# Optimization experiments

Measured on AMD Instinct MI355X. Metric: run time of the kernel, lower is better.

## Reference

```python
import jax, jax.numpy as jnp
import numpy as np

L, B, E, H = 1024, 8, 1024, 16
HD = E // H
SCALE = HD ** -0.5
EPS = 1e-5


def setup_inputs() -> dict:
    key = jax.random.key(0)
    ks = jax.random.split(key, 6)
    s = E ** -0.5
    return {
        "x": jax.random.normal(ks[0], (L, B, E), dtype=jnp.float32),
        "attn_mask": jnp.zeros((L, L), dtype=jnp.float32),
        "Wq": jax.random.normal(ks[1], (E, E), dtype=jnp.float32) * s,
        "bq": jnp.zeros((E,), dtype=jnp.float32),
        "Wk": jax.random.normal(ks[2], (E, E), dtype=jnp.float32) * s,
        "bk": jnp.zeros((E,), dtype=jnp.float32),
        "Wv": jax.random.normal(ks[3], (E, E), dtype=jnp.float32) * s,
        "bv": jnp.zeros((E,), dtype=jnp.float32),
        "Wo": jax.random.normal(ks[4], (E, E), dtype=jnp.float32) * s,
        "bo": jnp.zeros((E,), dtype=jnp.float32),
        "gamma": jnp.ones((E,), dtype=jnp.float32),
        "beta": jnp.zeros((E,), dtype=jnp.float32),
    }


def _layernorm(x, gamma, beta):
    mu = jnp.mean(x, axis=-1, keepdims=True)
    var = jnp.mean(jnp.square(x - mu), axis=-1, keepdims=True)
    return (x - mu) * jax.lax.rsqrt(var + EPS) * gamma + beta


def reference(x, attn_mask, Wq, bq, Wk, bk, Wv, bv, Wo, bo, gamma, beta):
    # x: (L, B, E); pre-LN residual attention block (dropout=0, eval)
    ln_x = _layernorm(x, gamma, beta)
    # torch Linear: y = x @ W.T + b
    q = (ln_x @ Wq.T + bq) * SCALE
    k = ln_x @ Wk.T + bk
    v = ln_x @ Wv.T + bv
    # (L, B, E) -> (B, H, L, hd)
    def split_heads(t):
        return t.reshape(L, B, H, HD).transpose(1, 2, 0, 3)
    q, k, v = split_heads(q), split_heads(k), split_heads(v)
    # full attention matrix, as in the original non-fused bmm path
    attn = jnp.einsum('bhqd,bhkd->bhqk', q, k) + attn_mask[None, None]
    attn = jax.nn.softmax(attn, axis=-1)
    out = jnp.einsum('bhqk,bhkd->bhqd', attn, v)  # (B, H, L, hd)
    out = out.transpose(2, 0, 1, 3).reshape(L, B, E)
    out = out @ Wo.T + bo
    return x + out
```

## Files before the change

kernel.cpp:

```cpp
#include <hip/hip_runtime.h>

#define LL 1024
#define BB 8
#define EE 1024
#define HH 16
#define HD 64
#define MROWS (LL*BB)

typedef __attribute__((ext_vector_type(8))) short short8v;
typedef __attribute__((ext_vector_type(4))) float f32x4;
typedef __attribute__((ext_vector_type(16))) float f32x16;

__device__ __forceinline__ unsigned short tobf(float f) {
    union { float f; unsigned u; } un; un.f = f;
    unsigned u = un.u;
    u += 0x7fffu + ((u >> 16) & 1u);
    return (unsigned short)(u >> 16);
}

__device__ __forceinline__ void load_lds16(const unsigned short* g, unsigned short* l) {
    __builtin_amdgcn_global_load_lds((const __attribute__((address_space(1))) unsigned int*)g,
                                     (__attribute__((address_space(3))) unsigned int*)l,
                                     16, 0, 0);
}

__global__ __launch_bounds__(256) void convw4_kernel(const float* __restrict__ w0,
                                                     const float* __restrict__ w1,
                                                     const float* __restrict__ w2,
                                                     const float* __restrict__ w3,
                                                     unsigned short* __restrict__ o0,
                                                     unsigned short* __restrict__ o1,
                                                     unsigned short* __restrict__ o2,
                                                     unsigned short* __restrict__ o3) {
    const float* w; unsigned short* o;
    switch (blockIdx.y) {
        case 0:  w = w0; o = o0; break;
        case 1:  w = w1; o = o1; break;
        case 2:  w = w2; o = o2; break;
        default: w = w3; o = o3; break;
    }
    int i = (blockIdx.x * 256 + threadIdx.x) * 4;
    float4 v = *(const float4*)&w[i];
    ushort4 r;
    r.x = tobf(v.x); r.y = tobf(v.y); r.z = tobf(v.z); r.w = tobf(v.w);
    *(ushort4*)&o[i] = r;
}

__global__ __launch_bounds__(256) void ln_kernel(const float* __restrict__ x,
                                                 const float* __restrict__ gamma,
                                                 const float* __restrict__ beta,
                                                 unsigned short* __restrict__ out) {
    const int row = blockIdx.x;
    const int tid = threadIdx.x;
    const float4 v = *(const float4*)&x[(size_t)row * EE + tid * 4];
    float s = v.x + v.y + v.z + v.w;
    float q = v.x*v.x + v.y*v.y + v.z*v.z + v.w*v.w;
    #pragma unroll
    for (int off = 1; off < 64; off <<= 1) {
        s += __shfl_xor(s, off);
        q += __shfl_xor(q, off);
    }
    __shared__ float ss[4], sq[4];
    const int wv = tid >> 6;
    if ((tid & 63) == 0) { ss[wv] = s; sq[wv] = q; }
    __syncthreads();
    s = ss[0] + ss[1] + ss[2] + ss[3];
    q = sq[0] + sq[1] + sq[2] + sq[3];
    const float mu = s * (1.0f / EE);
    const float var = q * (1.0f / EE) - mu * mu;
    const float rs = rsqrtf(var + 1e-5f);
    ushort4 o;
    o.x = tobf((v.x - mu) * rs * gamma[tid*4+0] + beta[tid*4+0]);
    o.y = tobf((v.y - mu) * rs * gamma[tid*4+1] + beta[tid*4+1]);
    o.z = tobf((v.z - mu) * rs * gamma[tid*4+2] + beta[tid*4+2]);
    o.w = tobf((v.w - mu) * rs * gamma[tid*4+3] + beta[tid*4+3]);
    *(ushort4*)&out[(size_t)row * EE + tid * 4] = o;
}

#define GEMM128_BODY(A_, W_)                                                              \
    __shared__ unsigned short a_sh[128*32];                                               \
    __shared__ unsigned short b_sh[128*32];                                               \
    const int tid = threadIdx.x, lane = tid & 63, wave = tid >> 6;                        \
    const int bm = blockIdx.y * 128, bn = blockIdx.x * 128;                               \
    const int wr = (wave >> 1) * 64, wc = (wave & 1) * 64;                                \
    const int l16 = lane & 15, lk8 = (lane >> 4) * 8;                                     \
    const int grow = lane >> 2, gcol = (lane & 3) * 8;                                    \
    f32x4 acc[4][4] = {};                                                                 \
    for (int k0 = 0; k0 < EE; k0 += 32) {                                                 \
        _Pragma("unroll")                                                                 \
        for (int i = 0; i < 2; ++i) {                                                     \
            const int c = wave * 2 + i;                                                   \
            load_lds16(&A_[(size_t)(bm + c*16 + grow)*EE + k0 + gcol], a_sh + c*512);     \
            load_lds16(&W_[(size_t)(bn + c*16 + grow)*EE + k0 + gcol], b_sh + c*512);     \
        }                                                                                 \
        __syncthreads();                                                                  \
        short8v af[4], bf[4];                                                             \
        _Pragma("unroll")                                                                 \
        for (int mi = 0; mi < 4; ++mi) af[mi] = *(const short8v*)&a_sh[(wr + mi*16 + l16)*32 + lk8]; \
        _Pragma("unroll")                                                                 \
        for (int ni = 0; ni < 4; ++ni) bf[ni] = *(const short8v*)&b_sh[(wc + ni*16 + l16)*32 + lk8]; \
        _Pragma("unroll")                                                                 \
        for (int mi = 0; mi < 4; ++mi)                                                    \
            _Pragma("unroll")                                                             \
            for (int ni = 0; ni < 4; ++ni)                                                \
                acc[mi][ni] = __builtin_amdgcn_mfma_f32_16x16x32_bf16(af[mi], bf[ni], acc[mi][ni], 0, 0, 0); \
        __syncthreads();                                                                  \
    }

__global__ __launch_bounds__(256) void gemm_qkv(const unsigned short* __restrict__ A,
                                                const unsigned short* __restrict__ W,
                                                const float* __restrict__ bq,
                                                const float* __restrict__ bk,
                                                const float* __restrict__ bv,
                                                unsigned short* __restrict__ qo,
                                                unsigned short* __restrict__ ko,
                                                unsigned short* __restrict__ vo) {
    GEMM128_BODY(A, W)
    const int seg = blockIdx.x >> 3;
    const float* bias = seg == 0 ? bq : (seg == 1 ? bk : bv);
    #pragma unroll
    for (int mi = 0; mi < 4; ++mi) {
        #pragma unroll
        for (int ni = 0; ni < 4; ++ni) {
            #pragma unroll
            for (int r = 0; r < 4; ++r) {
                const int m  = bm + wr + mi*16 + (lane >> 4)*4 + r;
                const int nn = (bn & 1023) + wc + ni*16 + l16;
                const float v = acc[mi][ni][r] + bias[nn];
                const int l = m >> 3, b = m & 7, h = nn >> 6, d = nn & 63;
                if (seg == 0)      qo[((size_t)(b*HH + h) * LL + l) * HD + d] = tobf(v * 0.125f);
                else if (seg == 1) ko[((size_t)(b*HH + h) * LL + l) * HD + d] = tobf(v);
                else               vo[((size_t)(b*HH + h) * HD + d) * LL + l] = tobf(v);
            }
        }
    }
}

__global__ __launch_bounds__(256) void gemm_o(const unsigned short* __restrict__ A,
                                              const unsigned short* __restrict__ W,
                                              const float* __restrict__ bias,
                                              const float* __restrict__ xres,
                                              float* __restrict__ outf) {
    GEMM128_BODY(A, W)
    #pragma unroll
    for (int mi = 0; mi < 4; ++mi) {
        #pragma unroll
        for (int ni = 0; ni < 4; ++ni) {
            #pragma unroll
            for (int r = 0; r < 4; ++r) {
                const int m = bm + wr + mi*16 + (lane >> 4)*4 + r;
                const int n = bn + wc + ni*16 + l16;
                outf[(size_t)m * EE + n] = acc[mi][ni][r] + bias[n] + xres[(size_t)m * EE + n];
            }
        }
    }
}

__global__ __launch_bounds__(256) void attn_kernel(const unsigned short* __restrict__ qarr,
                                                   const unsigned short* __restrict__ karr,
                                                   const unsigned short* __restrict__ vtarr,
                                                   const float* __restrict__ mask,
                                                   unsigned short* __restrict__ attn_out) {
    __shared__ __attribute__((aligned(16))) unsigned short k_sh[2][64*64];
    __shared__ __attribute__((aligned(16))) unsigned short v_sh[2][64*64];
    const int tid = threadIdx.x, lane = tid & 63, wave = tid >> 6;
    const int l32 = lane & 31, hi = lane >> 5;
    const int bh = blockIdx.y;
    const int qtok = blockIdx.x * 128 + wave * 32 + l32;
    const unsigned short* qb = qarr  + (size_t)bh * LL * HD;
    const unsigned short* kb = karr  + (size_t)bh * LL * HD;
    const unsigned short* vb = vtarr + (size_t)bh * HD * LL;

    short8v qf[4];
    #pragma unroll
    for (int dc = 0; dc < 4; ++dc)
        qf[dc] = *(const short8v*)&qb[(size_t)qtok * HD + dc*16 + hi*8];

    f32x16 acc[2] = {};
    float mrun = -1e30f, srun = 0.f;

    auto stage = [&](int buf, int kv) {
        #pragma unroll
        for (int i = 0; i < 2; ++i) {
            const int r = wave*16 + i*8 + (lane >> 3);
            const int c = ((lane & 7) ^ (r & 7)) * 8;
            load_lds16(&kb[(size_t)(kv + r) * HD + c], &k_sh[buf][(wave*16 + i*8) * 64]);
            load_lds16(&vb[(size_t)r * LL + kv + c],   &v_sh[buf][(wave*16 + i*8) * 64]);
        }
    };

    stage(0, 0);
    for (int t = 0; t < LL/64; ++t) {
        const int buf = t & 1;
        __syncthreads();
        if (t < LL/64 - 1) stage(buf ^ 1, (t + 1) * 64);

        #pragma unroll
        for (int sub = 0; sub < 2; ++sub) {
            f32x16 s = {};
            #pragma unroll
            for (int dc = 0; dc < 4; ++dc) {
                const int row = sub*32 + l32;
                const short8v kf = *(const short8v*)((const char*)&k_sh[buf][0]
                                     + (size_t)row*128 + (((dc*2 + hi) ^ (l32 & 7)) * 16));
                s = __builtin_amdgcn_mfma_f32_32x32x16_bf16(kf, qf[dc], s, 0, 0, 0);
            }
            const float* mrow = &mask[(size_t)qtok * LL + t*64 + sub*32 + hi*4];
            #pragma unroll
            for (int g = 0; g < 4; ++g) {
                const float4 mv = *(const float4*)&mrow[g*8];
                s[4*g+0] += mv.x; s[4*g+1] += mv.y; s[4*g+2] += mv.z; s[4*g+3] += mv.w;
            }
            float pm = s[0];
            #pragma unroll
            for (int i = 1; i < 16; ++i) pm = fmaxf(pm, s[i]);
            pm = fmaxf(pm, __shfl_xor(pm, 32));
            if (__any(pm - mrun > 8.0f)) {
                const float mn = fmaxf(mrun, pm);
                const float al = __expf(mrun - mn);
                #pragma unroll
                for (int i = 0; i < 16; ++i) { acc[0][i] *= al; acc[1][i] *= al; }
                srun *= al;
                mrun = mn;
            }
            float p[16]; float rs = 0.f;
            #pragma unroll
            for (int i = 0; i < 16; ++i) { p[i] = __expf(s[i] - mrun); rs += p[i]; }
            rs += __shfl_xor(rs, 32);
            srun += rs;
            unsigned w[8];
            #pragma unroll
            for (int j = 0; j < 8; ++j)
                asm("v_cvt_pk_bf16_f32 %0, %1, %2" : "=v"(w[j]) : "v"(p[2*j]), "v"(p[2*j+1]));
            asm volatile("v_permlane32_swap_b32 %0, %1" : "+v"(w[0]), "+v"(w[2]));
            asm volatile("v_permlane32_swap_b32 %0, %1" : "+v"(w[1]), "+v"(w[3]));
            asm volatile("v_permlane32_swap_b32 %0, %1" : "+v"(w[4]), "+v"(w[6]));
            asm volatile("v_permlane32_swap_b32 %0, %1" : "+v"(w[5]), "+v"(w[7]));
            union { uint4 u; short8v s8; } pb0, pb1;
            pb0.u = make_uint4(w[0], w[1], w[2], w[3]);
            pb1.u = make_uint4(w[4], w[5], w[6], w[7]);
            #pragma unroll
            for (int dt = 0; dt < 2; ++dt) {
                const int row = dt*32 + l32;
                const short8v vf0 = *(const short8v*)((const char*)&v_sh[buf][0]
                                      + (size_t)row*128 + ((((sub*2+0)*2 + hi) ^ (l32 & 7)) * 16));
                const short8v vf1 = *(const short8v*)((const char*)&v_sh[buf][0]
                                      + (size_t)row*128 + ((((sub*2+1)*2 + hi) ^ (l32 & 7)) * 16));
                acc[dt] = __builtin_amdgcn_mfma_f32_32x32x16_bf16(vf0, pb0.s8, acc[dt], 0, 0, 0);
                acc[dt] = __builtin_amdgcn_mfma_f32_32x32x16_bf16(vf1, pb1.s8, acc[dt], 0, 0, 0);
            }
        }
    }
    const float inv = 1.0f / srun;
    const int b = bh >> 4, h = bh & 15;
    unsigned short* orow = attn_out + ((size_t)qtok * BB + b) * EE + h * HD;
    #pragma unroll
    for (int dt = 0; dt < 2; ++dt) {
        #pragma unroll
        for (int g = 0; g < 4; ++g) {
            const float a0 = acc[dt][4*g+0]*inv, a1 = acc[dt][4*g+1]*inv;
            const float a2 = acc[dt][4*g+2]*inv, a3 = acc[dt][4*g+3]*inv;
            unsigned lo, hw;
            asm("v_cvt_pk_bf16_f32 %0, %1, %2" : "=v"(lo) : "v"(a0), "v"(a1));
            asm("v_cvt_pk_bf16_f32 %0, %1, %2" : "=v"(hw) : "v"(a2), "v"(a3));
            *(uint2*)&orow[dt*32 + g*8 + hi*4] = make_uint2(lo, hw);
        }
    }
}

extern "C" void kernel_launch(void* const* d_in, const int* in_sizes, int n_in,
                              void* d_out, int out_size, void* d_ws, size_t ws_size,
                              hipStream_t stream) {
    (void)in_sizes; (void)n_in; (void)out_size; (void)ws_size;
    const float* x     = (const float*)d_in[0];
    const float* mask  = (const float*)d_in[1];
    const float* Wq    = (const float*)d_in[2];
    const float* bq    = (const float*)d_in[3];
    const float* Wk    = (const float*)d_in[4];
    const float* bk    = (const float*)d_in[5];
    const float* Wv    = (const float*)d_in[6];
    const float* bv    = (const float*)d_in[7];
    const float* Wo    = (const float*)d_in[8];
    const float* bo    = (const float*)d_in[9];
    const float* gamma = (const float*)d_in[10];
    const float* beta  = (const float*)d_in[11];
    float* out = (float*)d_out;

    unsigned short* ws   = (unsigned short*)d_ws;
    unsigned short* ln   = ws;
    unsigned short* wqkv = ln   + (size_t)MROWS * EE;
    unsigned short* wob  = wqkv + (size_t)3 * EE * EE;
    unsigned short* qb   = wob  + (size_t)EE * EE;
    unsigned short* kbp  = qb   + (size_t)BB * HH * LL * HD;
    unsigned short* vtb  = kbp  + (size_t)BB * HH * LL * HD;
    unsigned short* attnb = ln;

    convw4_kernel<<<dim3(1024, 4), 256, 0, stream>>>(
        Wq, Wk, Wv, Wo,
        wqkv, wqkv + (size_t)EE * EE, wqkv + (size_t)2 * EE * EE, wob);
    ln_kernel<<<MROWS, 256, 0, stream>>>(x, gamma, beta, ln);

    gemm_qkv<<<dim3(24, 64), 256, 0, stream>>>(ln, wqkv, bq, bk, bv, qb, kbp, vtb);

    attn_kernel<<<dim3(LL / 128, BB * HH), 256, 0, stream>>>(qb, kbp, vtb, mask, attnb);

    gemm_o<<<dim3(8, 64), 256, 0, stream>>>(attnb, wob, bo, x, out);
}
```

Baseline: 232.8 us.

## Widen GEMM K-tile with swizzled LDS; use exp2 softmax with mask prefetch

The shared GEMM body now stages 64-wide K slices with an XOR-swizzled LDS layout, which halves the number of barrier iterations and avoids LDS bank conflicts. The attention kernel folds log2(e) into the Q scaling and the mask so it can use exp2f. It also prefetches the next mask slice into registers one step ahead, switches to tree reductions for the max and the sum, and raises wave priority around the MFMA blocks. These changes target barrier overhead, exp cost and mask load latency, at the price of more LDS and register use.

Result: no change. 228.9 us (-1.7%).

```diff
diff --git a/kernel.cpp b/kernel.cpp
--- a/kernel.cpp
+++ b/kernel.cpp
@@ -11,11 +11,17 @@
 typedef __attribute__((ext_vector_type(4))) float f32x4;
 typedef __attribute__((ext_vector_type(16))) float f32x16;
 
+#define LOG2E 1.44269504088896f
+
 __device__ __forceinline__ unsigned short tobf(float f) {
     union { float f; unsigned u; } un; un.f = f;
     unsigned u = un.u;
     u += 0x7fffu + ((u >> 16) & 1u);
     return (unsigned short)(u >> 16);
+}
+
+__device__ __forceinline__ float max3f(float a, float b, float c) {
+    return fmaxf(fmaxf(a, b), c);
 }
 
 __device__ __forceinline__ void load_lds16(const unsigned short* g, unsigned short* l) {
@@ -78,32 +84,40 @@
 }
 
 #define GEMM128_BODY(A_, W_)                                                              \
-    __shared__ unsigned short a_sh[128*32];                                               \
-    __shared__ unsigned short b_sh[128*32];                                               \
+    __shared__ unsigned short a_sh[128*64];                                               \
+    __shared__ unsigned short b_sh[128*64];                                               \
     const int tid = threadIdx.x, lane = tid & 63, wave = tid >> 6;                        \
     const int bm = blockIdx.y * 128, bn = blockIdx.x * 128;                               \
     const int wr = (wave >> 1) * 64, wc = (wave & 1) * 64;                                \
-    const int l16 = lane & 15, lk8 = (lane >> 4) * 8;                                     \
-    const int grow = lane >> 2, gcol = (lane & 3) * 8;                                    \
+    const int l16 = lane & 15, q4 = lane >> 4;                                            \
+    const int grow8 = lane >> 3;                                                          \
+    const int gsl = ((lane & 7) ^ grow8) * 8;                                             \
     f32x4 acc[4][4] = {};                                                                 \
-    for (int k0 = 0; k0 < EE; k0 += 32) {                                                 \
+    for (int k0 = 0; k0 < EE; k0 += 64) {                                                 \
         _Pragma("unroll")                                                                 \
-        for (int i = 0; i < 2; ++i) {                                                     \
-            const int c = wave * 2 + i;                                                   \
-            load_lds16(&A_[(size_t)(bm + c*16 + grow)*EE + k0 + gcol], a_sh + c*512);     \
-            load_lds16(&W_[(size_t)(bn + c*16 + grow)*EE + k0 + gcol], b_sh + c*512);     \
+        for (int i = 0; i < 4; ++i) {                                                     \
+            const int ch = wave * 4 + i;                                                  \
+            load_lds16(&A_[(size_t)(bm + ch*8 + grow8)*EE + k0 + gsl], a_sh + ch*512);    \
+            load_lds16(&W_[(size_t)(bn + ch*8 + grow8)*EE + k0 + gsl], b_sh + ch*512);    \
         }                                                                                 \
         __syncthreads();                                                                  \
-        short8v af[4], bf[4];                                                             \
         _Pragma("unroll")                                                                 \
-        for (int mi = 0; mi < 4; ++mi) af[mi] = *(const short8v*)&a_sh[(wr + mi*16 + l16)*32 + lk8]; \
-        _Pragma("unroll")                                                                 \
-        for (int ni = 0; ni < 4; ++ni) bf[ni] = *(const short8v*)&b_sh[(wc + ni*16 + l16)*32 + lk8]; \
-        _Pragma("unroll")                                                                 \
-        for (int mi = 0; mi < 4; ++mi)                                                    \
+        for (int kh = 0; kh < 2; ++kh) {                                                  \
+            short8v af[4], bf[4];                                                         \
+            _Pragma("unroll")                                                             \
+            for (int mi = 0; mi < 4; ++mi)                                                \
+                af[mi] = *(const short8v*)((const char*)a_sh                              \
+                           + (size_t)(wr + mi*16 + l16)*128 + (((kh*4 + q4) ^ (l16 & 7))*16)); \
             _Pragma("unroll")                                                             \
             for (int ni = 0; ni < 4; ++ni)                                                \
-                acc[mi][ni] = __builtin_amdgcn_mfma_f32_16x16x32_bf16(af[mi], bf[ni], acc[mi][ni], 0, 0, 0); \
+                bf[ni] = *(const short8v*)((const char*)b_sh                              \
+                           + (size_t)(wc + ni*16 + l16)*128 + (((kh*4 + q4) ^ (l16 & 7))*16)); \
+            _Pragma("unroll")                                                             \
+            for (int mi = 0; mi < 4; ++mi)                                                \
+                _Pragma("unroll")                                                         \
+                for (int ni = 0; ni < 4; ++ni)                                            \
+                    acc[mi][ni] = __builtin_amdgcn_mfma_f32_16x16x32_bf16(af[mi], bf[ni], acc[mi][ni], 0, 0, 0); \
+        }                                                                                 \
         __syncthreads();                                                                  \
     }
 
@@ -128,7 +142,7 @@
                 const int nn = (bn & 1023) + wc + ni*16 + l16;
                 const float v = acc[mi][ni][r] + bias[nn];
                 const int l = m >> 3, b = m & 7, h = nn >> 6, d = nn & 63;
-                if (seg == 0)      qo[((size_t)(b*HH + h) * LL + l) * HD + d] = tobf(v * 0.125f);
+                if (seg == 0)      qo[((size_t)(b*HH + h) * LL + l) * HD + d] = tobf(v * (0.125f * LOG2E));
                 else if (seg == 1) ko[((size_t)(b*HH + h) * LL + l) * HD + d] = tobf(v);
                 else               vo[((size_t)(b*HH + h) * HD + d) * LL + l] = tobf(v);
             }
@@ -189,6 +203,11 @@
         }
     };
 
+    const float* mbase = &mask[(size_t)qtok * LL + hi*4];
+    float4 mcur[4], mnxt[4];
+    #pragma unroll
+    for (int g = 0; g < 4; ++g) mcur[g] = *(const float4*)&mbase[g*8];
+
     stage(0, 0);
     for (int t = 0; t < LL/64; ++t) {
         const int buf = t & 1;
@@ -197,7 +216,15 @@
 
         #pragma unroll
         for (int sub = 0; sub < 2; ++sub) {
+            {
+                const int nt = (sub == 0) ? t : (t < LL/64 - 1 ? t + 1 : t);
+                const int ns = sub ^ 1;
+                const float* mrow = &mbase[(size_t)nt*64 + ns*32];
+                #pragma unroll
+                for (int g = 0; g < 4; ++g) mnxt[g] = *(const float4*)&mrow[g*8];
+            }
             f32x16 s = {};
+            __builtin_amdgcn_s_setprio(1);
             #pragma unroll
             for (int dc = 0; dc < 4; ++dc) {
                 const int row = sub*32 + l32;
@@ -205,27 +232,38 @@
                                      + (size_t)row*128 + (((dc*2 + hi) ^ (l32 & 7)) * 16));
                 s = __builtin_amdgcn_mfma_f32_32x32x16_bf16(kf, qf[dc], s, 0, 0, 0);
             }
-            const float* mrow = &mask[(size_t)qtok * LL + t*64 + sub*32 + hi*4];
+            __builtin_amdgcn_s_setprio(0);
             #pragma unroll
             for (int g = 0; g < 4; ++g) {
-                const float4 mv = *(const float4*)&mrow[g*8];
-                s[4*g+0] += mv.x; s[4*g+1] += mv.y; s[4*g+2] += mv.z; s[4*g+3] += mv.w;
-            }
-            float pm = s[0];
-            #pragma unroll
-            for (int i = 1; i < 16; ++i) pm = fmaxf(pm, s[i]);
+                s[4*g+0] = fmaf(mcur[g].x, LOG2E, s[4*g+0]);
+                s[4*g+1] = fmaf(mcur[g].y, LOG2E, s[4*g+1]);
+                s[4*g+2] = fmaf(mcur[g].z, LOG2E, s[4*g+2]);
+                s[4*g+3] = fmaf(mcur[g].w, LOG2E, s[4*g+3]);
+            }
+            #pragma unroll
+            for (int g = 0; g < 4; ++g) mcur[g] = mnxt[g];
+            const float a0 = max3f(s[0],  s[1],  s[2]);
+            const float a1 = max3f(s[3],  s[4],  s[5]);
+            const float a2 = max3f(s[6],  s[7],  s[8]);
+            const float a3 = max3f(s[9],  s[10], s[11]);
+            const float a4 = max3f(s[12], s[13], s[14]);
+            float pm = fmaxf(max3f(a0, a1, a2), max3f(a3, a4, s[15]));
             pm = fmaxf(pm, __shfl_xor(pm, 32));
             if (__any(pm - mrun > 8.0f)) {
                 const float mn = fmaxf(mrun, pm);
-                const float al = __expf(mrun - mn);
+                const float al = exp2f(mrun - mn);
                 #pragma unroll
                 for (int i = 0; i < 16; ++i) { acc[0][i] *= al; acc[1][i] *= al; }
                 srun *= al;
                 mrun = mn;
             }
-            float p[16]; float rs = 0.f;
-            #pragma unroll
-            for (int i = 0; i < 16; ++i) { p[i] = __expf(s[i] - mrun); rs += p[i]; }
+            float p[16];
+            #pragma unroll
+            for (int i = 0; i < 16; ++i) p[i] = exp2f(s[i] - mrun);
+            const float t0 = p[0]+p[1],   t1 = p[2]+p[3],   t2 = p[4]+p[5],   t3 = p[6]+p[7];
+            const float t4 = p[8]+p[9],   t5 = p[10]+p[11], t6 = p[12]+p[13], t7 = p[14]+p[15];
+            const float u0 = t0+t1, u1 = t2+t3, u2 = t4+t5, u3 = t6+t7;
+            float rs = (u0+u1) + (u2+u3);
             rs += __shfl_xor(rs, 32);
             srun += rs;
             unsigned w[8];
@@ -239,6 +277,7 @@
             union { uint4 u; short8v s8; } pb0, pb1;
             pb0.u = make_uint4(w[0], w[1], w[2], w[3]);
             pb1.u = make_uint4(w[4], w[5], w[6], w[7]);
+            __builtin_amdgcn_s_setprio(1);
             #pragma unroll
             for (int dt = 0; dt < 2; ++dt) {
                 const int row = dt*32 + l32;
@@ -249,6 +288,7 @@
                 acc[dt] = __builtin_amdgcn_mfma_f32_32x32x16_bf16(vf0, pb0.s8, acc[dt], 0, 0, 0);
                 acc[dt] = __builtin_amdgcn_mfma_f32_32x32x16_bf16(vf1, pb1.s8, acc[dt], 0, 0, 0);
             }
+            __builtin_amdgcn_s_setprio(0);
         }
     }
     const float inv = 1.0f / srun;
```
